# Kernel optimization log

Hardware: AMD Instinct MI355X
Metric: run time of the kernel (lower is better)

The kernel has to match this reference:

```python
import jax, jax.numpy as jnp
import numpy as np

N_TASK, N_WORKER, N_STATION = 20000, 5000, 1000
D, HEADS, LAYERS = 64, 4, 2
EDGE_COUNTS = [50000, 30000, 30000, 40000, 40000]
# (n_src, n_dst) per relation: precedes, assigned_to, has_task, can_do, done_by
EDGE_SPEC = [(N_TASK, N_TASK), (N_TASK, N_STATION), (N_STATION, N_TASK), (N_WORKER, N_TASK), (N_TASK, N_WORKER)]
EDGE_TYPES = [('task', 'task'), ('task', 'station'), ('station', 'task'), ('worker', 'task'), ('task', 'worker')]


def setup_inputs() -> dict:
    key = jax.random.key(0)
    ks = iter(jax.random.split(key, 64))
    inp = {}
    inp['x_task'] = jax.random.normal(next(ks), (N_TASK, 16), jnp.float32)
    inp['x_worker'] = jax.random.normal(next(ks), (N_WORKER, 12), jnp.float32)
    inp['x_station'] = jax.random.normal(next(ks), (N_STATION, 10), jnp.float32)
    for i, (E, (ns, nd)) in enumerate(zip(EDGE_COUNTS, EDGE_SPEC)):
        src = jax.random.randint(next(ks), (E,), 0, ns)
        dst = jax.random.randint(next(ks), (E,), 0, nd)
        inp[f'ei{i}'] = jnp.stack([src, dst]).astype(jnp.int32)
    def lin(k, i, o):
        return jax.random.normal(k, (i, o), jnp.float32) / np.float32(np.sqrt(i))
    # feature embedder params (Linear + LayerNorm affine) per node type
    for name, fd in [('task', 16), ('worker', 12), ('station', 10)]:
        inp[f'W_{name}'] = lin(next(ks), fd, D)
        inp[f'b_{name}'] = jnp.zeros((D,), jnp.float32)
        inp[f'g_{name}'] = jnp.ones((D,), jnp.float32)
        inp[f'beta_{name}'] = jnp.zeros((D,), jnp.float32)
    # stacked GATv2 params: [layers, 5 edge types, ...]
    inp['gat_Wl'] = jax.random.normal(next(ks), (LAYERS, 5, D, HEADS * D), jnp.float32) / np.float32(np.sqrt(D))
    inp['gat_Wr'] = jax.random.normal(next(ks), (LAYERS, 5, D, HEADS * D), jnp.float32) / np.float32(np.sqrt(D))
    inp['gat_att'] = jax.random.normal(next(ks), (LAYERS, 5, HEADS, D), jnp.float32) * np.float32(0.1)
    inp['gat_bias'] = jnp.zeros((LAYERS, 5, D), jnp.float32)
    return inp


def _layer_norm(x, g, b):
    m = x.mean(-1, keepdims=True)
    v = ((x - m) ** 2).mean(-1, keepdims=True)
    return (x - m) * jax.lax.rsqrt(v + 1e-5) * g + b


def _gatv2(x_src, x_dst, ei, Wl, Wr, att, bias):
    # GATv2Conv, concat=False (mean over heads), no self loops
    n_dst = x_dst.shape[0]
    xl = (x_src @ Wl).reshape(-1, HEADS, D)  # [Ns,H,Dh]
    xr = (x_dst @ Wr).reshape(-1, HEADS, D)  # [Nd,H,Dh]
    src, dst = ei[0], ei[1]
    e = jax.nn.leaky_relu(xl[src] + xr[dst], 0.2)          # [E,H,Dh]
    logits = jnp.einsum('ehd,hd->eh', e, att)              # [E,H]
    m = jax.ops.segment_max(logits, dst, num_segments=n_dst)
    ex = jnp.exp(logits - m[dst])
    denom = jax.ops.segment_sum(ex, dst, num_segments=n_dst)
    alpha = ex / denom[dst]                                # segment softmax per dst node
    out = jax.ops.segment_sum(alpha[..., None] * xl[src], dst, num_segments=n_dst)
    return out.mean(axis=1) + bias                         # [Nd,D]


def _forward(x_task, x_worker, x_station, eis,
             W_task, b_task, g_task, beta_task,
             W_worker, b_worker, g_worker, beta_worker,
             W_station, b_station, g_station, beta_station,
             gat_Wl, gat_Wr, gat_att, gat_bias):
    x = {
        'task': jax.nn.relu(_layer_norm(x_task @ W_task + b_task, g_task, beta_task)),
        'worker': jax.nn.relu(_layer_norm(x_worker @ W_worker + b_worker, g_worker, beta_worker)),
        'station': jax.nn.relu(_layer_norm(x_station @ W_station + b_station, g_station, beta_station)),
    }
    for l in range(LAYERS):
        agg = {'task': 0.0, 'worker': 0.0, 'station': 0.0}
        for t, (st, dt) in enumerate(EDGE_TYPES):
            agg[dt] = agg[dt] + _gatv2(x[st], x[dt], eis[t], gat_Wl[l, t], gat_Wr[l, t], gat_att[l, t], gat_bias[l, t])
        x = {k: jax.nn.relu(agg[k]) + x[k] for k in x}  # HeteroConv sum aggr, then ReLU + residual
    gc = jnp.concatenate([
        x['station'].mean(0), x['task'].mean(0), x['worker'].mean(0),
        x['station'].max(0), x['task'].max(0), x['worker'].max(0),
    ])[None, :]  # [1, 6*D]
    return x['task'], x['worker'], x['station'], gc


def reference(x_task, x_worker, x_station, ei0, ei1, ei2, ei3, ei4,
              W_task, b_task, g_task, beta_task,
              W_worker, b_worker, g_worker, beta_worker,
              W_station, b_station, g_station, beta_station,
              gat_Wl, gat_Wr, gat_att, gat_bias):
    return _forward(x_task, x_worker, x_station, (ei0, ei1, ei2, ei3, ei4),
                    W_task, b_task, g_task, beta_task,
                    W_worker, b_worker, g_worker, beta_worker,
                    W_station, b_station, g_station, beta_station,
                    gat_Wl, gat_Wr, gat_att, gat_bias)
```

## Files before the change

### kernel.cpp

```cpp
#include <hip/hip_runtime.h>
#include <math.h>

#define NT 20000
#define NW 5000
#define NS 1000

typedef __attribute__((ext_vector_type(8))) short bf16x8;
typedef __attribute__((ext_vector_type(4))) float f32x4;

#define CB_T 1250
#define CB_W 313
#define CB_S 63
#define CB_ALL 1626

struct GemmSeg { const short* X; const short* Wt; short* Y; int N; int blk0; };
struct GemmTab { GemmSeg s[10]; int nseg; };

struct GatSeg { const int* rowp; const int* col; const short* xl; const short* xr;
                const float* att; const float* bias; float* agg; int Nd; int wave0; };
struct GatTab { GatSeg s[5]; int nseg; };

struct EdgeSeg { const int* ei; int* cnt; int* col; int E; int blk0; };
struct EdgeTab { EdgeSeg s[5]; int nseg; };

struct ScanTab { int* cnt[5]; int* rowp[5]; int n[5]; };

struct Mega0 {
  const float *xT, *xW, *xS, *WT, *WW, *WS;
  const float *bT, *gT, *beT, *bW, *gW, *beW, *bS, *gS, *beS;
  float *yT, *yW, *yS; short *ybT, *ybW, *ybS;
  const float *gWl, *gWr; short *Wlt, *Wrt; int* nxtAll;
};

__device__ __forceinline__ float wsum64(float v) {
  #pragma unroll
  for (int o = 32; o > 0; o >>= 1) v += __shfl_xor(v, o, 64);
  return v;
}
__device__ __forceinline__ short f2b(float f) {
  unsigned u = __float_as_uint(f);
  unsigned r = (u + 0x7FFFu + ((u >> 16) & 1u)) >> 16;
  return (short)(unsigned short)r;
}
__device__ __forceinline__ float blo(unsigned x) { return __uint_as_float(x << 16); }
__device__ __forceinline__ float bhi(unsigned x) { return __uint_as_float(x & 0xFFFF0000u); }

__global__ void mega0_kernel(Mega0 M) {
  int b = blockIdx.x;
  if (b < 6500) {
    int gid = b * 256 + threadIdx.x;
    int wid = gid >> 6, lane = gid & 63;
    const float *x, *W, *bb, *gg, *be; float* y; short* yb; int FD, n;
    if (wid < NT)            { x = M.xT; W = M.WT; bb = M.bT; gg = M.gT; be = M.beT; y = M.yT; yb = M.ybT; FD = 16; n = wid; }
    else if (wid < NT + NW)  { x = M.xW; W = M.WW; bb = M.bW; gg = M.gW; be = M.beW; y = M.yW; yb = M.ybW; FD = 12; n = wid - NT; }
    else                     { x = M.xS; W = M.WS; bb = M.bS; gg = M.gS; be = M.beS; y = M.yS; yb = M.ybS; FD = 10; n = wid - NT - NW; }
    const float* xr = x + (size_t)n * FD;
    float acc = bb[lane];
    for (int k = 0; k < FD; ++k) acc = fmaf(xr[k], W[k * 64 + lane], acc);
    float m = wsum64(acc) * (1.f / 64.f);
    float d = acc - m;
    float v = wsum64(d * d) * (1.f / 64.f);
    float o = d * rsqrtf(v + 1e-5f) * gg[lane] + be[lane];
    o = fmaxf(o, 0.f);
    y[(size_t)n * 64 + lane] = o;
    yb[(size_t)n * 64 + lane] = f2b(o);
  } else {
    int idx = (b - 6500) * 256 + threadIdx.x;
    if (idx < 66000) M.nxtAll[idx] = 0;
    int side = idx >= 163840;
    int j = idx - side * 163840;
    int m = j >> 14, e = j & 16383;
    int k = e >> 8, colv = e & 255;
    const float* src = side ? M.gWr : M.gWl;
    short* dst = side ? M.Wrt : M.Wlt;
    dst[m * 16384 + colv * 64 + k] = f2b(src[m * 16384 + e]);
  }
}

__global__ void count_kernel(EdgeTab tab) {
  int b = blockIdx.x, si = 0;
  for (int i = 1; i < tab.nseg; ++i) if (b >= tab.s[i].blk0) si = i;
  EdgeSeg sg = tab.s[si];
  int e = (b - sg.blk0) * 256 + threadIdx.x;
  if (e < sg.E) atomicAdd(&sg.cnt[sg.ei[sg.E + e]], 1);
}

__global__ void scan_kernel(ScanTab tab) {
  int t = blockIdx.x;
  int* cnt = tab.cnt[t]; int* rowp = tab.rowp[t]; int n = tab.n[t];
  __shared__ int wsums[16];
  __shared__ int carry_s;
  int tid = threadIdx.x, lane = tid & 63, w = tid >> 6;
  if (tid == 0) carry_s = 0;
  __syncthreads();
  for (int base = 0; base < n; base += 1024) {
    int i = base + tid;
    int v = (i < n) ? cnt[i] : 0;
    int s = v;
    #pragma unroll
    for (int o = 1; o < 64; o <<= 1) { int x = __shfl_up(s, o, 64); if (lane >= o) s += x; }
    if (lane == 63) wsums[w] = s;
    __syncthreads();
    if (w == 0 && lane < 16) {
      int x = wsums[lane];
      #pragma unroll
      for (int o = 1; o < 16; o <<= 1) { int y = __shfl_up(x, o, 16); if (lane >= o) x += y; }
      wsums[lane] = x;
    }
    __syncthreads();
    int carry   = carry_s;
    int waveoff = (w == 0) ? 0 : wsums[w - 1];
    int exc     = carry + waveoff + s - v;
    if (i < n) { rowp[i] = exc; cnt[i] = exc; }
    __syncthreads();
    if (tid == 0) carry_s += wsums[15];
    __syncthreads();
  }
  if (threadIdx.x == 0) rowp[n] = carry_s;
}

__global__ void fill_kernel(EdgeTab tab) {
  int b = blockIdx.x, si = 0;
  for (int i = 1; i < tab.nseg; ++i) if (b >= tab.s[i].blk0) si = i;
  EdgeSeg sg = tab.s[si];
  int e = (b - sg.blk0) * 256 + threadIdx.x;
  if (e >= sg.E) return;
  int s = sg.ei[e], d = sg.ei[sg.E + e];
  int pos = atomicAdd(&sg.cnt[d], 1);
  sg.col[pos] = s;
}

__global__ __launch_bounds__(256) void gemm_kernel(GemmTab tab) {
  __shared__ short lds[4096 + 16896];
  int b = blockIdx.x, si = 0;
  for (int i = 1; i < tab.nseg; ++i) if (b >= tab.s[i].blk0) si = i;
  GemmSeg sg = tab.s[si];
  int r0 = (b - sg.blk0) * 64;
  int tid = threadIdx.x;
  #pragma unroll
  for (int it = 0; it < 2; ++it) {
    int idx = it * 256 + tid;
    int row = idx >> 3, kq = idx & 7;
    bf16x8 v = {0, 0, 0, 0, 0, 0, 0, 0};
    if (r0 + row < sg.N) v = *(const bf16x8*)&sg.X[(size_t)(r0 + row) * 64 + kq * 8];
    *(bf16x8*)&lds[(row * 8 + (kq ^ (row & 7))) * 8] = v;
  }
  #pragma unroll
  for (int it = 0; it < 8; ++it) {
    int idx = it * 256 + tid;
    int col = idx >> 3, kq = idx & 7;
    bf16x8 v = *(const bf16x8*)&sg.Wt[col * 64 + kq * 8];
    *(bf16x8*)&lds[4096 + (col * 8 + (kq ^ (col & 7))) * 8] = v;
  }
  __syncthreads();
  int lane = tid & 63, wv = tid >> 6;
  int r = lane & 15, hk = lane >> 4;
  f32x4 acc[4][4];
  #pragma unroll
  for (int rt = 0; rt < 4; ++rt)
    #pragma unroll
    for (int ct = 0; ct < 4; ++ct) acc[rt][ct] = (f32x4){0.f, 0.f, 0.f, 0.f};
  #pragma unroll
  for (int kk = 0; kk < 2; ++kk) {
    int kq = kk * 4 + hk;
    bf16x8 a[4], bb[4];
    #pragma unroll
    for (int rt = 0; rt < 4; ++rt) {
      int row = rt * 16 + r;
      a[rt] = *(const bf16x8*)&lds[(row * 8 + (kq ^ (row & 7))) * 8];
    }
    #pragma unroll
    for (int ct = 0; ct < 4; ++ct) {
      int col = wv * 64 + ct * 16 + r;
      bb[ct] = *(const bf16x8*)&lds[4096 + (col * 8 + (kq ^ (col & 7))) * 8];
    }
    #pragma unroll
    for (int rt = 0; rt < 4; ++rt)
      #pragma unroll
      for (int ct = 0; ct < 4; ++ct)
        acc[rt][ct] = __builtin_amdgcn_mfma_f32_16x16x32_bf16(a[rt], bb[ct], acc[rt][ct], 0, 0, 0);
  }
  __syncthreads();
  #pragma unroll
  for (int rt = 0; rt < 4; ++rt)
    #pragma unroll
    for (int j = 0; j < 4; ++j) {
      int rowl = rt * 16 + hk * 4 + j;
      #pragma unroll
      for (int ct = 0; ct < 4; ++ct)
        lds[rowl * 264 + wv * 64 + ct * 16 + r] = f2b(acc[rt][ct][j]);
    }
  __syncthreads();
  #pragma unroll
  for (int it = 0; it < 8; ++it) {
    int idx = it * 256 + tid;
    int row = idx >> 5, v8 = idx & 31;
    if (r0 + row < sg.N) {
      bf16x8 v = *(const bf16x8*)&lds[row * 264 + v8 * 8];
      *(bf16x8*)&sg.Y[(size_t)(r0 + row) * 256 + v8 * 8] = v;
    }
  }
}

__global__ void gat_kernel(GatTab tab) {
  int gwave = (blockIdx.x * blockDim.x + threadIdx.x) >> 6;
  int lane  = threadIdx.x & 63;
  int si = 0;
  for (int i = 1; i < tab.nseg; ++i) if (gwave >= tab.s[i].wave0) si = i;
  GatSeg sg = tab.s[si];
  int n = gwave - sg.wave0;
  if (n >= sg.Nd) return;
  int h = lane >> 4, lig = lane & 15;
  int beg = sg.rowp[n], end = sg.rowp[n + 1];
  uint2 xru = *(const uint2*)&sg.xr[(size_t)n * 256 + h * 64 + lig * 4];
  float4 a4 = *(const float4*)&sg.att[h * 64 + lig * 4];
  float xr0 = blo(xru.x), xr1 = bhi(xru.x), xr2 = blo(xru.y), xr3 = bhi(xru.y);
  float den = 0.f, c0 = 0.f, c1 = 0.f, c2 = 0.f, c3 = 0.f;
  if (end > beg) {
    int sNxt = sg.col[beg];
    uint2 w = *(const uint2*)&sg.xl[(size_t)sNxt * 256 + h * 64 + lig * 4];
    if (beg + 1 < end) sNxt = sg.col[beg + 1];
    for (int i = beg; i < end; ++i) {
      uint2 wc = w;
      if (i + 1 < end)
        w = *(const uint2*)&sg.xl[(size_t)sNxt * 256 + h * 64 + lig * 4];
      if (i + 2 < end) sNxt = sg.col[i + 2];
      float f0 = blo(wc.x), f1 = bhi(wc.x), f2v = blo(wc.y), f3 = bhi(wc.y);
      float vx = f0 + xr0, vy = f1 + xr1, vz = f2v + xr2, vw = f3 + xr3;
      vx = fmaxf(vx, 0.2f * vx); vy = fmaxf(vy, 0.2f * vy);
      vz = fmaxf(vz, 0.2f * vz); vw = fmaxf(vw, 0.2f * vw);
      float dd = fmaf(vx, a4.x, fmaf(vy, a4.y, fmaf(vz, a4.z, vw * a4.w)));
      dd += __shfl_xor(dd, 1, 64);
      dd += __shfl_xor(dd, 2, 64);
      dd += __shfl_xor(dd, 4, 64);
      dd += __shfl_xor(dd, 8, 64);
      float e = __expf(dd);
      den += e;
      c0 = fmaf(e, f0, c0); c1 = fmaf(e, f1, c1);
      c2 = fmaf(e, f2v, c2); c3 = fmaf(e, f3, c3);
    }
  }
  float o0 = 0.f, o1 = 0.f, o2 = 0.f, o3 = 0.f;
  if (end > beg) {
    float inv = 1.f / den;
    o0 = c0 * inv; o1 = c1 * inv; o2 = c2 * inv; o3 = c3 * inv;
  }
  o0 += __shfl_xor(o0, 16, 64); o0 += __shfl_xor(o0, 32, 64);
  o1 += __shfl_xor(o1, 16, 64); o1 += __shfl_xor(o1, 32, 64);
  o2 += __shfl_xor(o2, 16, 64); o2 += __shfl_xor(o2, 32, 64);
  o3 += __shfl_xor(o3, 16, 64); o3 += __shfl_xor(o3, 32, 64);
  if (lane < 16) {
    float4 b4 = *(const float4*)&sg.bias[lane * 4];
    float4 res;
    res.x = fmaf(0.25f, o0, b4.x); res.y = fmaf(0.25f, o1, b4.y);
    res.z = fmaf(0.25f, o2, b4.z); res.w = fmaf(0.25f, o3, b4.w);
    *(float4*)&sg.agg[(size_t)n * 64 + lane * 4] = res;
  }
}

template <int POOL>
__global__ __launch_bounds__(256) void combine_kernel(
    const float4* __restrict__ aT0, const float4* __restrict__ aT2, const float4* __restrict__ aT3,
    const float4* __restrict__ aW, const float4* __restrict__ aS,
    const float4* __restrict__ xT, const float4* __restrict__ xW, const float4* __restrict__ xS,
    float4* __restrict__ oT, float4* __restrict__ oW, float4* __restrict__ oS,
    unsigned* __restrict__ bT, unsigned* __restrict__ bW, unsigned* __restrict__ bS,
    float4* __restrict__ psum, float4* __restrict__ pmax) {
  int b = blockIdx.x, tid = threadIdx.x;
  const float4 *a, *x; float4* o; unsigned* bo; int n4, local; bool sum3 = false;
  const float4 *a2 = nullptr, *a3 = nullptr;
  if (b < CB_T)              { a = aT0; a2 = aT2; a3 = aT3; x = xT; o = oT; bo = bT; n4 = NT * 16; local = b; sum3 = true; }
  else if (b < CB_T + CB_W)  { a = aW; x = xW; o = oW; bo = bW; n4 = NW * 16; local = b - CB_T; }
  else                       { a = aS; x = xS; o = oS; bo = bS; n4 = NS * 16; local = b - CB_T - CB_W; }
  int j = local * 256 + tid;
  bool valid = j < n4;
  float4 r = make_float4(0.f, 0.f, 0.f, 0.f);
  if (valid) {
    float4 av = a[j];
    if (sum3) {
      float4 v2 = a2[j], v3 = a3[j];
      av.x += v2.x + v3.x; av.y += v2.y + v3.y; av.z += v2.z + v3.z; av.w += v2.w + v3.w;
    }
    float4 xv = x[j];
    r.x = fmaxf(av.x, 0.f) + xv.x; r.y = fmaxf(av.y, 0.f) + xv.y;
    r.z = fmaxf(av.z, 0.f) + xv.z; r.w = fmaxf(av.w, 0.f) + xv.w;
    o[j] = r;
    if (POOL == 0 && bo) {
      unsigned lo = (unsigned)(unsigned short)f2b(r.x) | ((unsigned)(unsigned short)f2b(r.y) << 16);
      unsigned hi = (unsigned)(unsigned short)f2b(r.z) | ((unsigned)(unsigned short)f2b(r.w) << 16);
      bo[j * 2] = lo; bo[j * 2 + 1] = hi;
    }
  }
  if (POOL) {
    float4 s = r;
    float4 m = valid ? r : make_float4(-3e38f, -3e38f, -3e38f, -3e38f);
    #pragma unroll
    for (int off = 16; off <= 32; off <<= 1) {
      s.x += __shfl_xor(s.x, off, 64); s.y += __shfl_xor(s.y, off, 64);
      s.z += __shfl_xor(s.z, off, 64); s.w += __shfl_xor(s.w, off, 64);
      m.x = fmaxf(m.x, __shfl_xor(m.x, off, 64)); m.y = fmaxf(m.y, __shfl_xor(m.y, off, 64));
      m.z = fmaxf(m.z, __shfl_xor(m.z, off, 64)); m.w = fmaxf(m.w, __shfl_xor(m.w, off, 64));
    }
    __shared__ float4 ls[4][16], lm[4][16];
    int w = tid >> 6, q = tid & 15;
    if (((tid >> 4) & 3) == 0) { ls[w][q] = s; lm[w][q] = m; }
    __syncthreads();
    if (tid < 16) {
      float4 S = ls[0][tid], M = lm[0][tid];
      #pragma unroll
      for (int i = 1; i < 4; ++i) {
        float4 s2 = ls[i][tid], m2 = lm[i][tid];
        S.x += s2.x; S.y += s2.y; S.z += s2.z; S.w += s2.w;
        M.x = fmaxf(M.x, m2.x); M.y = fmaxf(M.y, m2.y);
        M.z = fmaxf(M.z, m2.z); M.w = fmaxf(M.w, m2.w);
      }
      psum[b * 16 + tid] = S;
      pmax[b * 16 + tid] = M;
    }
  }
}

__global__ void pool2_kernel(const float* __restrict__ psum,
                             const float* __restrict__ pmax,
                             float* __restrict__ gc) {
  int b = blockIdx.x;
  int lane = threadIdx.x & 63, w = threadIdx.x >> 6;
  int off, cnt, N, mi;
  if (b == 0)      { off = CB_T + CB_W; cnt = CB_S; N = NS; mi = 0;   }
  else if (b == 1) { off = 0;           cnt = CB_T; N = NT; mi = 64;  }
  else             { off = CB_T;        cnt = CB_W; N = NW; mi = 128; }
  float s = 0.f, mx = -3e38f;
  for (int i = w; i < cnt; i += 16) {
    s += psum[(size_t)(off + i) * 64 + lane];
    mx = fmaxf(mx, pmax[(size_t)(off + i) * 64 + lane]);
  }
  __shared__ float ss[16][64], sm[16][64];
  ss[w][lane] = s; sm[w][lane] = mx;
  __syncthreads();
  if (w == 0) {
    #pragma unroll
    for (int i = 1; i < 16; ++i) { s += ss[i][lane]; mx = fmaxf(mx, sm[i][lane]); }
    gc[mi + lane] = s / (float)N;
    gc[192 + mi + lane] = mx;
  }
}

extern "C" void kernel_launch(void* const* d_in, const int* in_sizes, int n_in,
                              void* d_out, int out_size, void* d_ws, size_t ws_size,
                              hipStream_t stream) {
  const float* x_in[3] = {(const float*)d_in[0], (const float*)d_in[1], (const float*)d_in[2]};
  const int*   ei[5]   = {(const int*)d_in[3], (const int*)d_in[4], (const int*)d_in[5],
                          (const int*)d_in[6], (const int*)d_in[7]};
  const float* Wemb[3] = {(const float*)d_in[8],  (const float*)d_in[12], (const float*)d_in[16]};
  const float* bemb[3] = {(const float*)d_in[9],  (const float*)d_in[13], (const float*)d_in[17]};
  const float* gemb[3] = {(const float*)d_in[10], (const float*)d_in[14], (const float*)d_in[18]};
  const float* beemb[3]= {(const float*)d_in[11], (const float*)d_in[15], (const float*)d_in[19]};
  const float* gWl   = (const float*)d_in[20];
  const float* gWr   = (const float*)d_in[21];
  const float* gatt  = (const float*)d_in[22];
  const float* gbias = (const float*)d_in[23];

  const int NN[3]  = {NT, NW, NS};
  const int EC[5]  = {50000, 30000, 30000, 40000, 40000};
  const int STy[5] = {0, 0, 2, 1, 0};
  const int DTy[5] = {0, 2, 0, 0, 1};

  char* p = (char*)d_ws;
  auto alloc = [&](size_t bytes) -> void* {
    void* r = (void*)p;
    p += (bytes + 255) & ~(size_t)255;
    return r;
  };
  float* xc[3];  short* xcb[3];
  for (int k = 0; k < 3; ++k) xc[k]  = (float*)alloc((size_t)NN[k] * 64 * 4);
  for (int k = 0; k < 3; ++k) xcb[k] = (short*)alloc((size_t)NN[k] * 64 * 2);
  float* aggT0 = (float*)alloc((size_t)NT * 64 * 4);
  float* aggT2 = (float*)alloc((size_t)NT * 64 * 4);
  float* aggT3 = (float*)alloc((size_t)NT * 64 * 4);
  float* aggW  = (float*)alloc((size_t)NW * 64 * 4);
  float* aggS  = (float*)alloc((size_t)NS * 64 * 4);
  float* aggOf[5] = {aggT0, aggS, aggT2, aggT3, aggW};
  int* nxtAll = (int*)alloc((size_t)66000 * 4);
  int  nxtOff[5] = {0, NT, NT + NS, 2 * NT + NS, 3 * NT + NS};
  int* nxt[5]; for (int t = 0; t < 5; ++t) nxt[t] = nxtAll + nxtOff[t];
  int *rowp[5], *col[5];
  for (int t = 0; t < 5; ++t) {
    rowp[t] = (int*)alloc((size_t)(NN[DTy[t]] + 1) * 4);
    col[t]  = (int*)alloc((size_t)EC[t] * 4);
  }
  float* psum = (float*)alloc((size_t)CB_ALL * 64 * 4);
  float* pmax = (float*)alloc((size_t)CB_ALL * 64 * 4);
  short* Wlt  = (short*)alloc((size_t)10 * 16384 * 2);
  short* Wrt  = (short*)alloc((size_t)10 * 16384 * 2);
  short *xlT[5], *xrT[5];
  for (int t = 0; t < 5; ++t) {
    xlT[t] = (short*)alloc((size_t)NN[STy[t]] * 256 * 2);
    xrT[t] = (short*)alloc((size_t)NN[DTy[t]] * 256 * 2);
  }

  EdgeTab etab; etab.nseg = 5;
  int eb = 0;
  for (int t = 0; t < 5; ++t) {
    etab.s[t] = {ei[t], nxt[t], col[t], EC[t], eb};
    eb += (EC[t] + 255) / 256;
  }

  Mega0 M;
  M.xT = x_in[0]; M.xW = x_in[1]; M.xS = x_in[2];
  M.WT = Wemb[0]; M.WW = Wemb[1]; M.WS = Wemb[2];
  M.bT = bemb[0]; M.gT = gemb[0]; M.beT = beemb[0];
  M.bW = bemb[1]; M.gW = gemb[1]; M.beW = beemb[1];
  M.bS = bemb[2]; M.gS = gemb[2]; M.beS = beemb[2];
  M.yT = xc[0]; M.yW = xc[1]; M.yS = xc[2];
  M.ybT = xcb[0]; M.ybW = xcb[1]; M.ybS = xcb[2];
  M.gWl = gWl; M.gWr = gWr; M.Wlt = Wlt; M.Wrt = Wrt; M.nxtAll = nxtAll;
  mega0_kernel<<<7780, 256, 0, stream>>>(M);

  count_kernel<<<eb, 256, 0, stream>>>(etab);
  ScanTab stab;
  for (int t = 0; t < 5; ++t) { stab.cnt[t] = nxt[t]; stab.rowp[t] = rowp[t]; stab.n[t] = NN[DTy[t]]; }
  scan_kernel<<<5, 1024, 0, stream>>>(stab);
  fill_kernel<<<eb, 256, 0, stream>>>(etab);

  float* outT = (float*)d_out;
  float* outW = outT + (size_t)NT * 64;
  float* outS = outW + (size_t)NW * 64;
  float* gc   = outS + (size_t)NS * 64;

  for (int l = 0; l < 2; ++l) {
    GemmTab gt; gt.nseg = 10;
    int gb = 0;
    for (int t = 0; t < 5; ++t) {
      size_t off = (size_t)(l * 5 + t);
      gt.s[2 * t + 0] = {xcb[STy[t]], Wlt + off * 16384, xlT[t], NN[STy[t]], gb};
      gb += (NN[STy[t]] + 63) / 64;
      gt.s[2 * t + 1] = {xcb[DTy[t]], Wrt + off * 16384, xrT[t], NN[DTy[t]], gb};
      gb += (NN[DTy[t]] + 63) / 64;
    }
    gemm_kernel<<<gb, 256, 0, stream>>>(gt);

    GatTab at; at.nseg = 5;
    const int order[5] = {1, 4, 0, 2, 3};
    int wv = 0;
    for (int oi = 0; oi < 5; ++oi) {
      int t = order[oi];
      size_t off = (size_t)(l * 5 + t);
      at.s[oi] = {rowp[t], col[t], xlT[t], xrT[t], gatt + off * 256, gbias + off * 64,
                  aggOf[t], NN[DTy[t]], wv};
      wv += NN[DTy[t]];
    }
    gat_kernel<<<(wv * 64) / 256, 256, 0, stream>>>(at);

    if (l == 0) {
      combine_kernel<0><<<CB_ALL, 256, 0, stream>>>(
          (const float4*)aggT0, (const float4*)aggT2, (const float4*)aggT3,
          (const float4*)aggW, (const float4*)aggS,
          (const float4*)xc[0], (const float4*)xc[1], (const float4*)xc[2],
          (float4*)xc[0], (float4*)xc[1], (float4*)xc[2],
          (unsigned*)xcb[0], (unsigned*)xcb[1], (unsigned*)xcb[2],
          nullptr, nullptr);
    } else {
      combine_kernel<1><<<CB_ALL, 256, 0, stream>>>(
          (const float4*)aggT0, (const float4*)aggT2, (const float4*)aggT3,
          (const float4*)aggW, (const float4*)aggS,
          (const float4*)xc[0], (const float4*)xc[1], (const float4*)xc[2],
          (float4*)outT, (float4*)outW, (float4*)outS,
          nullptr, nullptr, nullptr,
          (float4*)psum, (float4*)pmax);
    }
  }

  pool2_kernel<<<3, 1024, 0, stream>>>(psum, pmax, gc);
}
```

Measured before the change: 227.6 us.

## Keep residual node state only in bf16 and vectorize CSR scan

Drops the fp32 copy of node embeddings so the embedder and the layer-0 combine write only bf16, and the residual add reads bf16 instead of fp32. This removes fp32 stores and loads of the node state between stages. It also makes the prefix scan handle four counts per thread with int4 loads and stores. The residual path now carries bf16 rounding error into the final outputs, and the scan assumes every node count is divisible by four.

```diff
diff --git a/kernel.cpp b/kernel.cpp
--- a/kernel.cpp
+++ b/kernel.cpp
@@ -28,7 +28,7 @@
 struct Mega0 {
   const float *xT, *xW, *xS, *WT, *WW, *WS;
   const float *bT, *gT, *beT, *bW, *gW, *beW, *bS, *gS, *beS;
-  float *yT, *yW, *yS; short *ybT, *ybW, *ybS;
+  short *ybT, *ybW, *ybS;
   const float *gWl, *gWr; short *Wlt, *Wrt; int* nxtAll;
 };
 
@@ -50,10 +50,10 @@
   if (b < 6500) {
     int gid = b * 256 + threadIdx.x;
     int wid = gid >> 6, lane = gid & 63;
-    const float *x, *W, *bb, *gg, *be; float* y; short* yb; int FD, n;
-    if (wid < NT)            { x = M.xT; W = M.WT; bb = M.bT; gg = M.gT; be = M.beT; y = M.yT; yb = M.ybT; FD = 16; n = wid; }
-    else if (wid < NT + NW)  { x = M.xW; W = M.WW; bb = M.bW; gg = M.gW; be = M.beW; y = M.yW; yb = M.ybW; FD = 12; n = wid - NT; }
-    else                     { x = M.xS; W = M.WS; bb = M.bS; gg = M.gS; be = M.beS; y = M.yS; yb = M.ybS; FD = 10; n = wid - NT - NW; }
+    const float *x, *W, *bb, *gg, *be; short* yb; int FD, n;
+    if (wid < NT)            { x = M.xT; W = M.WT; bb = M.bT; gg = M.gT; be = M.beT; yb = M.ybT; FD = 16; n = wid; }
+    else if (wid < NT + NW)  { x = M.xW; W = M.WW; bb = M.bW; gg = M.gW; be = M.beW; yb = M.ybW; FD = 12; n = wid - NT; }
+    else                     { x = M.xS; W = M.WS; bb = M.bS; gg = M.gS; be = M.beS; yb = M.ybS; FD = 10; n = wid - NT - NW; }
     const float* xr = x + (size_t)n * FD;
     float acc = bb[lane];
     for (int k = 0; k < FD; ++k) acc = fmaf(xr[k], W[k * 64 + lane], acc);
@@ -62,7 +62,6 @@
     float v = wsum64(d * d) * (1.f / 64.f);
     float o = d * rsqrtf(v + 1e-5f) * gg[lane] + be[lane];
     o = fmaxf(o, 0.f);
-    y[(size_t)n * 64 + lane] = o;
     yb[(size_t)n * 64 + lane] = f2b(o);
   } else {
     int idx = (b - 6500) * 256 + threadIdx.x;
@@ -87,16 +86,21 @@
 
 __global__ void scan_kernel(ScanTab tab) {
   int t = blockIdx.x;
-  int* cnt = tab.cnt[t]; int* rowp = tab.rowp[t]; int n = tab.n[t];
+  int4* cnt4  = (int4*)tab.cnt[t];
+  int*  rowp  = tab.rowp[t];
+  int4* rowp4 = (int4*)rowp;
+  int n  = tab.n[t];
+  int n4 = n >> 2;
   __shared__ int wsums[16];
   __shared__ int carry_s;
   int tid = threadIdx.x, lane = tid & 63, w = tid >> 6;
   if (tid == 0) carry_s = 0;
   __syncthreads();
-  for (int base = 0; base < n; base += 1024) {
+  for (int base = 0; base < n4; base += 1024) {
     int i = base + tid;
-    int v = (i < n) ? cnt[i] : 0;
-    int s = v;
+    int4 v = (i < n4) ? cnt4[i] : make_int4(0, 0, 0, 0);
+    int tsum = v.x + v.y + v.z + v.w;
+    int s = tsum;
     #pragma unroll
     for (int o = 1; o < 64; o <<= 1) { int x = __shfl_up(s, o, 64); if (lane >= o) s += x; }
     if (lane == 63) wsums[w] = s;
@@ -110,8 +114,13 @@
     __syncthreads();
     int carry   = carry_s;
     int waveoff = (w == 0) ? 0 : wsums[w - 1];
-    int exc     = carry + waveoff + s - v;
-    if (i < n) { rowp[i] = exc; cnt[i] = exc; }
+    int b0      = carry + waveoff + s - tsum;
+    if (i < n4) {
+      int4 e;
+      e.x = b0; e.y = b0 + v.x; e.z = e.y + v.y; e.w = e.z + v.z;
+      rowp4[i] = e;
+      cnt4[i]  = e;
+    }
     __syncthreads();
     if (tid == 0) carry_s += wsums[15];
     __syncthreads();
@@ -262,12 +271,12 @@
 __global__ __launch_bounds__(256) void combine_kernel(
     const float4* __restrict__ aT0, const float4* __restrict__ aT2, const float4* __restrict__ aT3,
     const float4* __restrict__ aW, const float4* __restrict__ aS,
-    const float4* __restrict__ xT, const float4* __restrict__ xW, const float4* __restrict__ xS,
+    const uint2* __restrict__ xT, const uint2* __restrict__ xW, const uint2* __restrict__ xS,
     float4* __restrict__ oT, float4* __restrict__ oW, float4* __restrict__ oS,
-    unsigned* __restrict__ bT, unsigned* __restrict__ bW, unsigned* __restrict__ bS,
+    uint2* __restrict__ bT, uint2* __restrict__ bW, uint2* __restrict__ bS,
     float4* __restrict__ psum, float4* __restrict__ pmax) {
   int b = blockIdx.x, tid = threadIdx.x;
-  const float4 *a, *x; float4* o; unsigned* bo; int n4, local; bool sum3 = false;
+  const float4 *a; const uint2* x; float4* o; uint2* bo; int n4, local; bool sum3 = false;
   const float4 *a2 = nullptr, *a3 = nullptr;
   if (b < CB_T)              { a = aT0; a2 = aT2; a3 = aT3; x = xT; o = oT; bo = bT; n4 = NT * 16; local = b; sum3 = true; }
   else if (b < CB_T + CB_W)  { a = aW; x = xW; o = oW; bo = bW; n4 = NW * 16; local = b - CB_T; }
@@ -281,14 +290,16 @@
       float4 v2 = a2[j], v3 = a3[j];
       av.x += v2.x + v3.x; av.y += v2.y + v3.y; av.z += v2.z + v3.z; av.w += v2.w + v3.w;
     }
-    float4 xv = x[j];
-    r.x = fmaxf(av.x, 0.f) + xv.x; r.y = fmaxf(av.y, 0.f) + xv.y;
-    r.z = fmaxf(av.z, 0.f) + xv.z; r.w = fmaxf(av.w, 0.f) + xv.w;
-    o[j] = r;
-    if (POOL == 0 && bo) {
-      unsigned lo = (unsigned)(unsigned short)f2b(r.x) | ((unsigned)(unsigned short)f2b(r.y) << 16);
-      unsigned hi = (unsigned)(unsigned short)f2b(r.z) | ((unsigned)(unsigned short)f2b(r.w) << 16);
-      bo[j * 2] = lo; bo[j * 2 + 1] = hi;
+    uint2 xv = x[j];
+    r.x = fmaxf(av.x, 0.f) + blo(xv.x); r.y = fmaxf(av.y, 0.f) + bhi(xv.x);
+    r.z = fmaxf(av.z, 0.f) + blo(xv.y); r.w = fmaxf(av.w, 0.f) + bhi(xv.y);
+    if (POOL == 0) {
+      uint2 pk;
+      pk.x = (unsigned)(unsigned short)f2b(r.x) | ((unsigned)(unsigned short)f2b(r.y) << 16);
+      pk.y = (unsigned)(unsigned short)f2b(r.z) | ((unsigned)(unsigned short)f2b(r.w) << 16);
+      bo[j] = pk;
+    } else {
+      o[j] = r;
     }
   }
   if (POOL) {
@@ -371,8 +382,7 @@
     p += (bytes + 255) & ~(size_t)255;
     return r;
   };
-  float* xc[3];  short* xcb[3];
-  for (int k = 0; k < 3; ++k) xc[k]  = (float*)alloc((size_t)NN[k] * 64 * 4);
+  short* xcb[3];
   for (int k = 0; k < 3; ++k) xcb[k] = (short*)alloc((size_t)NN[k] * 64 * 2);
   float* aggT0 = (float*)alloc((size_t)NT * 64 * 4);
   float* aggT2 = (float*)alloc((size_t)NT * 64 * 4);
@@ -411,7 +421,6 @@
   M.bT = bemb[0]; M.gT = gemb[0]; M.beT = beemb[0];
   M.bW = bemb[1]; M.gW = gemb[1]; M.beW = beemb[1];
   M.bS = bemb[2]; M.gS = gemb[2]; M.beS = beemb[2];
-  M.yT = xc[0]; M.yW = xc[1]; M.yS = xc[2];
   M.ybT = xcb[0]; M.ybW = xcb[1]; M.ybS = xcb[2];
   M.gWl = gWl; M.gWr = gWr; M.Wlt = Wlt; M.Wrt = Wrt; M.nxtAll = nxtAll;
   mega0_kernel<<<7780, 256, 0, stream>>>(M);
@@ -455,15 +464,15 @@
       combine_kernel<0><<<CB_ALL, 256, 0, stream>>>(
           (const float4*)aggT0, (const float4*)aggT2, (const float4*)aggT3,
           (const float4*)aggW, (const float4*)aggS,
-          (const float4*)xc[0], (const float4*)xc[1], (const float4*)xc[2],
-          (float4*)xc[0], (float4*)xc[1], (float4*)xc[2],
-          (unsigned*)xcb[0], (unsigned*)xcb[1], (unsigned*)xcb[2],
+          (const uint2*)xcb[0], (const uint2*)xcb[1], (const uint2*)xcb[2],
+          nullptr, nullptr, nullptr,
+          (uint2*)xcb[0], (uint2*)xcb[1], (uint2*)xcb[2],
           nullptr, nullptr);
     } else {
       combine_kernel<1><<<CB_ALL, 256, 0, stream>>>(
           (const float4*)aggT0, (const float4*)aggT2, (const float4*)aggT3,
           (const float4*)aggW, (const float4*)aggS,
-          (const float4*)xc[0], (const float4*)xc[1], (const float4*)xc[2],
+          (const uint2*)xcb[0], (const uint2*)xcb[1], (const uint2*)xcb[2],
           (float4*)outT, (float4*)outW, (float4*)outS,
           nullptr, nullptr, nullptr,
           (float4*)psum, (float4*)pmax);
```

After: 212.4 us. 6.7% less time.
